# Kernel tuning notes

Hardware: AMD Instinct MI355X
Metric: run time of the kernel (lower is better)

Reference implementation:

```python
import jax, jax.numpy as jnp
import numpy as np

BATCH, SEQ, D_IN, D_HID, D_OUT = 256, 512, 128, 128, 128


def setup_inputs() -> dict:
    key = jax.random.key(0)
    ks = jax.random.split(key, 10)
    def xavier(k, shape):
        std = (2.0 / (shape[0] + shape[1])) ** 0.5
        return jax.random.normal(k, shape, dtype=jnp.float32) * std
    return {
        "x": jax.random.normal(ks[0], (BATCH, SEQ, D_IN), dtype=jnp.float32),
        "x2i": xavier(ks[1], (D_IN, D_HID)),
        "x2f": xavier(ks[2], (D_IN, D_HID)),
        "x2g": xavier(ks[3], (D_IN, D_HID)),
        "x2o": xavier(ks[4], (D_IN, D_HID)),
        "h2i": xavier(ks[5], (D_HID, D_HID)),
        "h2f": xavier(ks[6], (D_HID, D_HID)),
        "h2g": xavier(ks[7], (D_HID, D_HID)),
        "h2o": xavier(ks[8], (D_HID, D_HID)),
        "w_out": xavier(ks[9], (D_HID, D_OUT)),
    }


def reference(x, x2i, x2f, x2g, x2o, h2i, h2f, h2g, h2o, w_out):
    batch = x.shape[0]
    hid = h2i.shape[0]
    # Precompute input projections for all timesteps (same math, hoisted out
    # of the recurrence): [B, S, 4H] -> time-major [S, B, 4H]
    wx = jnp.concatenate([x2i, x2f, x2g, x2o], axis=1)       # [D_IN, 4H]
    wh = jnp.concatenate([h2i, h2f, h2g, h2o], axis=1)       # [H, 4H]
    xg = jnp.einsum("bsi,ik->sbk", x, wx)                    # [S, B, 4H]

    def step(carry, xg_t):
        c, h = carry
        gates = xg_t + h @ wh                                # [B, 4H]
        i = jax.nn.sigmoid(gates[:, 0 * hid:1 * hid])
        f = jax.nn.sigmoid(gates[:, 1 * hid:2 * hid])
        g = jnp.tanh(gates[:, 2 * hid:3 * hid])
        o = jax.nn.sigmoid(gates[:, 3 * hid:4 * hid])
        c = f * c + i * g
        h = o * jnp.tanh(c)
        return (c, h), None

    c0 = jnp.zeros((batch, hid), dtype=x.dtype)
    h0 = jnp.zeros((batch, hid), dtype=x.dtype)
    (c_T, h_T), _ = jax.lax.scan(step, (c0, h0), xg)
    return h_T @ w_out
```

## Files before the change

kernel.cpp:

```cpp
#include <hip/hip_runtime.h>

typedef unsigned int u32;
typedef __fp16 half2_t __attribute__((ext_vector_type(2)));
typedef __fp16 half8_t __attribute__((ext_vector_type(8)));
typedef float  f32x4   __attribute__((ext_vector_type(4)));
typedef int    i32x4   __attribute__((ext_vector_type(4)));

#define DIN 128
#define DH  128
#define SEQL 512
#define NBATCH 256
#define NC  512
#define TC  64
#define NCHUNK (SEQL/TC)

#define HOFF 131072
#define HF2  (131072 + 256)
#define LDS_TOTAL (131072 + 256 + 256)

__device__ __forceinline__ u32 pk2(float a, float b) {
  half2_t h = __builtin_amdgcn_cvt_pkrtz(a, b);
  return __builtin_bit_cast(u32, h);
}

__device__ __forceinline__ float fexp2(float x) {
#if defined(__has_builtin) && __has_builtin(__builtin_amdgcn_exp2f)
  return __builtin_amdgcn_exp2f(x);
#else
  return __builtin_exp2f(x);
#endif
}

#define MF(A, B, C) __builtin_amdgcn_mfma_f32_16x16x32_f16( \
    __builtin_bit_cast(half8_t, A), __builtin_bit_cast(half8_t, B), C, 0, 0, 0)
#define MFI8(A, B, C) __builtin_amdgcn_mfma_i32_16x16x64_i8( \
    __builtin_bit_cast(i32x4, A), __builtin_bit_cast(i32x4, B), C, 0, 0, 0)

__global__ void pack_w(const float* __restrict__ x2i, const float* __restrict__ x2f,
                       const float* __restrict__ x2g, const float* __restrict__ x2o,
                       u32* __restrict__ wxT) {
  int idx = blockIdx.x * blockDim.x + threadIdx.x;
  if (idx >= NC * 64) return;
  int j = idx >> 6, kk = idx & 63;
  int g = j >> 7, jjj = j & 127;
  const float* wx = (g == 0) ? x2i : (g == 1) ? x2f : (g == 2) ? x2g : x2o;
  float s = (g == 2) ? -2.885390082f : -1.442695041f;
  wxT[idx] = pk2(s * wx[(2*kk)*DH + jjj], s * wx[(2*kk+1)*DH + jjj]);
}

__global__ void pack_whi8(const float* __restrict__ h2i, const float* __restrict__ h2f,
                          const float* __restrict__ h2g, const float* __restrict__ h2o,
                          u32* __restrict__ whI, float* __restrict__ dqs) {
  int j = blockIdx.x * blockDim.x + threadIdx.x;
  if (j >= NC) return;
  int g = j >> 7, jj = j & 127;
  const float* wh = (g == 0) ? h2i : (g == 1) ? h2f : (g == 2) ? h2g : h2o;
  float amax = 1e-20f;
  for (int k = 0; k < DH; ++k) amax = fmaxf(amax, fabsf(wh[k*DH + jj]));
  float s = 127.f / amax;
  for (int kk = 0; kk < 32; ++kk) {
    u32 wword = 0;
#pragma unroll
    for (int t = 0; t < 4; ++t) {
      int q = (int)__builtin_rintf(wh[(4*kk + t)*DH + jj] * s);
      wword |= ((u32)(q & 0xFF)) << (8 * t);
    }
    whI[j*32 + kk] = wword;
  }
  dqs[j] = (amax / 16129.f) * ((g == 2) ? -2.885390082f : -1.442695041f);
}

__global__ __launch_bounds__(512, 2)
void lstm_fused(
    const float* __restrict__ x, const u32* __restrict__ wxT,
    const u32* __restrict__ whI, const float* __restrict__ dqs,
    const float* __restrict__ w_out, float* __restrict__ out) {
  extern __shared__ char lds[];

  const int tid = threadIdx.x;
  const int b   = blockIdx.x;
  const int l   = tid & 63, wv = tid >> 6;
  const int kg  = l >> 4, r15 = l & 15;
  const int j   = wv * 16 + r15;

  uint4 bi8[4][2];
  float dqv[4];
#pragma unroll
  for (int g = 0; g < 4; ++g) {
    const uint4* wp = (const uint4*)(whI + (g * DH + j) * 32);
    bi8[g][0] = wp[kg];
    bi8[g][1] = wp[4 + kg];
    dqv[g] = dqs[g * DH + j];
  }
  uint4 bfA[4][4];
#pragma unroll
  for (int nt = 0; nt < 4; ++nt) {
    int n = wv * 64 + nt * 16 + r15;
#pragma unroll
    for (int ko = 0; ko < 4; ++ko)
      bfA[nt][ko] = *(const uint4*)(wxT + n*64 + ko*16 + kg*4);
  }

  if (tid < 64) ((u32*)(lds + HOFF))[tid] = 0u;
  float c = 0.f, lasth = 0.f;
  u32 rdh = HOFF;
  u32 wrh = HOFF + 128;
  const float* xb = x + (size_t)b * SEQL * DIN;
  const f32x4 Z  = {0.f, 0.f, 0.f, 0.f};
  const i32x4 ZI = {0, 0, 0, 0};
  __syncthreads();

#pragma unroll 1
  for (int tt = 0; tt < 4; ++tt) {
    uint4 afr0[4];
#pragma unroll
    for (int ko = 0; ko < 4; ++ko) {
      const float4* xp = (const float4*)(xb + (size_t)(tt*16 + r15)*DIN + ko*32 + kg*8);
      float4 v0 = xp[0], v1 = xp[1];
      afr0[ko].x = pk2(v0.x, v0.y); afr0[ko].y = pk2(v0.z, v0.w);
      afr0[ko].z = pk2(v1.x, v1.y); afr0[ko].w = pk2(v1.z, v1.w);
    }
#pragma unroll
    for (int nt = 0; nt < 4; ++nt) {
      int n = wv * 64 + nt * 16 + r15;
      f32x4 acc = MF(afr0[0], bfA[nt][0], Z);
      acc = MF(afr0[1], bfA[nt][1], acc);
      acc = MF(afr0[2], bfA[nt][2], acc);
      acc = MF(afr0[3], bfA[nt][3], acc);
      int t0 = tt*16 + kg*4;
      u32 off = (u32)(n*128 + ((t0*2) ^ ((n & 7) << 4)));
      uint2 pw; pw.x = pk2(acc[0], acc[1]); pw.y = pk2(acc[2], acc[3]);
      *(uint2*)(lds + off) = pw;
    }
  }
  __syncthreads();

  int cur = 0;
#pragma unroll 1
  for (int ch = 0; ch < NCHUNK; ++ch) {
    char* xgC = lds + cur * 65536;
    char* xgN = lds + (cur ^ 1) * 65536;
    const bool doA = (ch + 1 < NCHUNK);
    float4 lv[8];
    uint4  afr[4];
    f32x4  aacc;

#pragma unroll 1
    for (int m = 0; m < 8; ++m) {
      const int tt = m >> 1;
      half8_t xh[4];
#pragma unroll
      for (int g = 0; g < 4; ++g) {
        int cg = g * DH + j;
        xh[g] = __builtin_bit_cast(half8_t,
            *(const uint4*)(xgC + cg*128 + ((m*16) ^ ((cg & 7) << 4))));
      }
#pragma unroll
      for (int s8 = 0; s8 < 8; ++s8) {
        if (doA) {
          if ((m & 1) == 0) {
            if (s8 == 0) {
              const float* xr = xb + (size_t)((ch+1)*TC + tt*16 + r15)*DIN + kg*8;
#pragma unroll
              for (int ko = 0; ko < 4; ++ko) {
                const float4* xp = (const float4*)(xr + ko*32);
                lv[2*ko]   = xp[0];
                lv[2*ko+1] = xp[1];
              }
            }
            if (s8 == 2) {
#pragma unroll
              for (int ko = 0; ko < 2; ++ko) {
                float4 v0 = lv[2*ko], v1 = lv[2*ko+1];
                afr[ko].x = pk2(v0.x, v0.y); afr[ko].y = pk2(v0.z, v0.w);
                afr[ko].z = pk2(v1.x, v1.y); afr[ko].w = pk2(v1.z, v1.w);
              }
            }
            if (s8 == 3) {
#pragma unroll
              for (int ko = 2; ko < 4; ++ko) {
                float4 v0 = lv[2*ko], v1 = lv[2*ko+1];
                afr[ko].x = pk2(v0.x, v0.y); afr[ko].y = pk2(v0.z, v0.w);
                afr[ko].z = pk2(v1.x, v1.y); afr[ko].w = pk2(v1.z, v1.w);
              }
            }
          } else {
            const int nt = s8 >> 1;
            if ((s8 & 1) == 0) {
              aacc = MF(afr[1], bfA[nt][1], MF(afr[0], bfA[nt][0], Z));
            } else {
              aacc = MF(afr[3], bfA[nt][3], MF(afr[2], bfA[nt][2], aacc));
              int n = wv * 64 + nt * 16 + r15;
              int t0 = tt*16 + kg*4;
              u32 off = (u32)(n*128 + ((t0*2) ^ ((n & 7) << 4)));
              uint2 pw; pw.x = pk2(aacc[0], aacc[1]); pw.y = pk2(aacc[2], aacc[3]);
              *(uint2*)(xgN + off) = pw;
            }
          }
        }

        uint4 a0 = *(const uint4*)(lds + rdh + kg*16);
        uint4 a1 = *(const uint4*)(lds + rdh + 64 + kg*16);
        i32x4 aci = MFI8(a0, bi8[0][0], ZI);
        i32x4 acf = MFI8(a0, bi8[1][0], ZI);
        i32x4 acg = MFI8(a0, bi8[2][0], ZI);
        i32x4 aco = MFI8(a0, bi8[3][0], ZI);
        aci = MFI8(a1, bi8[0][1], aci);
        acf = MFI8(a1, bi8[1][1], acf);
        acg = MFI8(a1, bi8[2][1], acg);
        aco = MFI8(a1, bi8[3][1], aco);
        float gi = __builtin_fmaf((float)aci[0], dqv[0], (float)xh[0][s8]);
        float gf = __builtin_fmaf((float)acf[0], dqv[1], (float)xh[1][s8]);
        float gg = __builtin_fmaf((float)acg[0], dqv[2], (float)xh[2][s8]);
        float go = __builtin_fmaf((float)aco[0], dqv[3], (float)xh[3][s8]);
        float si = __builtin_amdgcn_rcpf(1.f + fexp2(gi));
        float sf = __builtin_amdgcn_rcpf(1.f + fexp2(gf));
        float sg = __builtin_fmaf(2.f, __builtin_amdgcn_rcpf(1.f + fexp2(gg)), -1.f);
        float so = __builtin_amdgcn_rcpf(1.f + fexp2(go));
        c = __builtin_fmaf(sf, c, si * sg);
        float th = __builtin_fmaf(2.f,
                     __builtin_amdgcn_rcpf(1.f + fexp2(c * -2.885390082f)), -1.f);
        float hval = so * th;
        lasth = hval;
        int q = (int)__builtin_rintf(hval * 127.f);
        if (l < 16) *(char*)(lds + wrh + j) = (char)q;
        u32 tswap = rdh; rdh = wrh; wrh = tswap;
        __syncthreads();
      }
    }
    cur ^= 1;
  }

  if (l < 16) *(__fp16*)(lds + HF2 + j * 2) = (__fp16)lasth;
  __syncthreads();
  if (tid < DH) {
    int n = tid;
    const u32* hf = (const u32*)(lds + HF2);
    float acc = 0.f;
#pragma unroll 8
    for (int kk = 0; kk < 64; ++kk) {
      half2_t h2v = __builtin_bit_cast(half2_t, hf[kk]);
      acc = __builtin_fmaf((float)h2v[0], w_out[(2*kk)*DH + n],
            __builtin_fmaf((float)h2v[1], w_out[(2*kk+1)*DH + n], acc));
    }
    out[b * DH + n] = acc;
  }
}

extern "C" void kernel_launch(void* const* d_in, const int* in_sizes, int n_in,
                              void* d_out, int out_size, void* d_ws, size_t ws_size,
                              hipStream_t stream) {
  const float* x    = (const float*)d_in[0];
  const float* x2i  = (const float*)d_in[1];
  const float* x2f  = (const float*)d_in[2];
  const float* x2g  = (const float*)d_in[3];
  const float* x2o  = (const float*)d_in[4];
  const float* h2i  = (const float*)d_in[5];
  const float* h2f  = (const float*)d_in[6];
  const float* h2g  = (const float*)d_in[7];
  const float* h2o  = (const float*)d_in[8];
  const float* wout = (const float*)d_in[9];

  u32*   wxT = (u32*)d_ws;
  u32*   whI = wxT + NC * 64;
  float* dqs = (float*)(whI + NC * 32);

  (void)hipFuncSetAttribute((const void*)lstm_fused,
                            hipFuncAttributeMaxDynamicSharedMemorySize, LDS_TOTAL);

  pack_w<<<64, 512, 0, stream>>>(x2i, x2f, x2g, x2o, wxT);
  pack_whi8<<<1, 512, 0, stream>>>(h2i, h2f, h2g, h2o, whI, dqs);
  lstm_fused<<<NBATCH, 512, LDS_TOTAL, stream>>>(x, wxT, whI, dqs, wout, (float*)d_out);
}
```

Measured before the change: 255.8 us.

## Distribute gate activations across lane groups and use a lighter step barrier

Each 16-lane group (kg) now computes the activation for only one of the four gates, then exchanges results with cross-lane shuffles. Before, every lane evaluated all four sigmoids and loaded all four xg fragments. This cuts the transcendental work and the LDS xg reads on the serial recurrence critical path, at the cost of three shuffles per step. It also swaps __syncthreads for an explicit lgkmcnt wait plus s_barrier, aiming to avoid extra waits on outstanding global loads. The c state is now only correct in lanes with kg==0. That is fine because only those lanes write h, though lanes in the other groups compute garbage c values.

```diff
diff --git a/kernel.cpp b/kernel.cpp
--- a/kernel.cpp
+++ b/kernel.cpp
@@ -29,6 +29,12 @@
 #else
   return __builtin_exp2f(x);
 #endif
+}
+
+__device__ __forceinline__ void step_barrier() {
+  asm volatile("s_waitcnt lgkmcnt(0)" ::: "memory");
+  __builtin_amdgcn_s_barrier();
+  asm volatile("" ::: "memory");
 }
 
 #define MF(A, B, C) __builtin_amdgcn_mfma_f32_16x16x32_f16( \
@@ -84,14 +90,15 @@
   const int j   = wv * 16 + r15;
 
   uint4 bi8[4][2];
-  float dqv[4];
 #pragma unroll
   for (int g = 0; g < 4; ++g) {
     const uint4* wp = (const uint4*)(whI + (g * DH + j) * 32);
     bi8[g][0] = wp[kg];
     bi8[g][1] = wp[4 + kg];
-    dqv[g] = dqs[g * DH + j];
-  }
+  }
+  const float dqo = dqs[kg * DH + j];
+  const float cA = (kg == 2) ? 2.f : 1.f;
+  const float cB = (kg == 2) ? -1.f : 0.f;
   uint4 bfA[4][4];
 #pragma unroll
   for (int nt = 0; nt < 4; ++nt) {
@@ -148,13 +155,9 @@
 #pragma unroll 1
     for (int m = 0; m < 8; ++m) {
       const int tt = m >> 1;
-      half8_t xh[4];
-#pragma unroll
-      for (int g = 0; g < 4; ++g) {
-        int cg = g * DH + j;
-        xh[g] = __builtin_bit_cast(half8_t,
-            *(const uint4*)(xgC + cg*128 + ((m*16) ^ ((cg & 7) << 4))));
-      }
+      const int cg = kg * DH + j;
+      half8_t xh = __builtin_bit_cast(half8_t,
+          *(const uint4*)(xgC + cg*128 + ((m*16) ^ ((cg & 7) << 4))));
 #pragma unroll
       for (int s8 = 0; s8 < 8; ++s8) {
         if (doA) {
@@ -209,23 +212,23 @@
         acf = MFI8(a1, bi8[1][1], acf);
         acg = MFI8(a1, bi8[2][1], acg);
         aco = MFI8(a1, bi8[3][1], aco);
-        float gi = __builtin_fmaf((float)aci[0], dqv[0], (float)xh[0][s8]);
-        float gf = __builtin_fmaf((float)acf[0], dqv[1], (float)xh[1][s8]);
-        float gg = __builtin_fmaf((float)acg[0], dqv[2], (float)xh[2][s8]);
-        float go = __builtin_fmaf((float)aco[0], dqv[3], (float)xh[3][s8]);
-        float si = __builtin_amdgcn_rcpf(1.f + fexp2(gi));
-        float sf = __builtin_amdgcn_rcpf(1.f + fexp2(gf));
-        float sg = __builtin_fmaf(2.f, __builtin_amdgcn_rcpf(1.f + fexp2(gg)), -1.f);
-        float so = __builtin_amdgcn_rcpf(1.f + fexp2(go));
-        c = __builtin_fmaf(sf, c, si * sg);
+        int aown = (kg == 0) ? aci[0] : (kg == 1) ? acf[0]
+                 : (kg == 2) ? acg[0] : aco[0];
+        float g0 = __builtin_fmaf((float)aown, dqo, (float)xh[s8]);
+        float y  = __builtin_amdgcn_rcpf(1.f + fexp2(g0));
+        float s  = __builtin_fmaf(cA, y, cB);
+        float sf_ = __shfl_xor(s, 16, 64);
+        float sg_ = __shfl_xor(s, 32, 64);
+        float so_ = __shfl_xor(s, 48, 64);
+        c = __builtin_fmaf(sf_, c, s * sg_);
         float th = __builtin_fmaf(2.f,
                      __builtin_amdgcn_rcpf(1.f + fexp2(c * -2.885390082f)), -1.f);
-        float hval = so * th;
+        float hval = so_ * th;
         lasth = hval;
         int q = (int)__builtin_rintf(hval * 127.f);
         if (l < 16) *(char*)(lds + wrh + j) = (char)q;
         u32 tswap = rdh; rdh = wrh; wrh = tswap;
-        __syncthreads();
+        step_barrier();
       }
     }
     cur ^= 1;
```

Result: no change. 258.9 us (+1.2%).
